# Performance work log

Measured on AMD Instinct MI355X. Metric: run time of the kernel, lower is better.

Reference implementation:

```python
import jax, jax.numpy as jnp
import numpy as np

V, E = 50000, 800000
NODE_IN, EDGE_IN, OUT, HEADS = 128, 16, 32, 4
NEG_SLOPE = 0.2  # DGL EdgeGATConv default negative_slope


def setup_inputs() -> dict:
    key = jax.random.key(0)
    ks = jax.random.split(key, 10)
    return {
        "node_feats": jax.random.normal(ks[0], (V, NODE_IN), jnp.float32),
        "edge_feats": jax.random.normal(ks[1], (E, EDGE_IN), jnp.float32),
        "src": jax.random.randint(ks[2], (E,), 0, V),
        "dst": jax.random.randint(ks[3], (E,), 0, V),
        "W_node": jax.random.normal(ks[4], (NODE_IN, HEADS * OUT), jnp.float32) * 0.05,
        "W_edge": jax.random.normal(ks[5], (EDGE_IN, HEADS * OUT), jnp.float32) * 0.05,
        "attn_l": jax.random.normal(ks[6], (HEADS, OUT), jnp.float32) * 0.05,
        "attn_r": jax.random.normal(ks[7], (HEADS, OUT), jnp.float32) * 0.05,
        "attn_e": jax.random.normal(ks[8], (HEADS, OUT), jnp.float32) * 0.05,
        "res_W": jax.random.normal(ks[9], (NODE_IN, HEADS * OUT), jnp.float32) * 0.05,
        "bias": jnp.zeros((HEADS * OUT,), jnp.float32),
    }


def _leaky_relu(x, slope):
    return jnp.where(x >= 0, x, slope * x)


def reference(node_feats, edge_feats, src, dst, W_node, W_edge, attn_l, attn_r, attn_e, res_W, bias):
    V = node_feats.shape[0]
    H, F = attn_l.shape
    # linear projections
    ft = (node_feats @ W_node).reshape(V, H, F)    # [V,H,F]
    fe = (edge_feats @ W_edge).reshape(-1, H, F)   # [E,H,F]
    # per-head attention logits
    el = jnp.einsum('vhf,hf->vh', ft, attn_l)      # [V,H]
    er = jnp.einsum('vhf,hf->vh', ft, attn_r)      # [V,H]
    ee = jnp.einsum('ehf,hf->eh', fe, attn_e)      # [E,H]
    e = _leaky_relu(el[src] + er[dst] + ee, NEG_SLOPE)  # [E,H]
    # edge softmax over incoming edges of each destination node (stable)
    emax = jax.ops.segment_max(e, dst, num_segments=V)  # [V,H]
    ex = jnp.exp(e - emax[dst])
    esum = jax.ops.segment_sum(ex, dst, num_segments=V)  # [V,H]
    a = ex / esum[dst]                                   # [E,H]
    # weighted message passing: u_mul_e(ft, a) then sum to dst
    msg = ft[src] * a[:, :, None]                        # [E,H,F]
    rst = jax.ops.segment_sum(msg, dst, num_segments=V)  # [V,H,F]
    # residual connection + bias (EdgeGATConv residual=True, bias=True)
    rst = rst + (node_feats @ res_W).reshape(V, H, F)
    rst = rst + bias.reshape(1, H, F)
    # agg_mode='flatten': concat heads
    return rst.reshape(V, H * F)
```

## Files before the change

### kernel.cpp

```cpp
#include <hip/hip_runtime.h>
#include <cstdint>

#define V_N 50000
#define E_N 800000
#define NODE_IN 128
#define EDGE_IN 16
#define HF 128
#define NEG_SLOPE 0.2f
#define NB_SCAN 196

#define OFF_FT    0
#define OFF_EL    3200000
#define OFF_ER    3400000
#define OFF_DEGP  3600000
#define OFF_ROW   4400000
#define OFF_BSUM  4450004
#define OFF_RANK  4450260
#define OFF_REC   5250260
#define OFF_WATT  8450260
#define OFF_BFRAG 8450324

typedef short bf16x8 __attribute__((ext_vector_type(8)));
typedef float f32x4 __attribute__((ext_vector_type(4)));

__device__ __forceinline__ unsigned short f2bf(float f) {
    unsigned u = __float_as_uint(f);
    u += 0x7fffu + ((u >> 16) & 1u);
    return (unsigned short)(u >> 16);
}
__device__ __forceinline__ unsigned pk2(float lo, float hi) {
    return (unsigned)f2bf(lo) | ((unsigned)f2bf(hi) << 16);
}
__device__ __forceinline__ float bflo(unsigned w) { return __uint_as_float(w << 16); }
__device__ __forceinline__ float bfhi(unsigned w) { return __uint_as_float(w & 0xffff0000u); }

__global__ void k_prep(const float* __restrict__ We,
                       const float* __restrict__ attn_e,
                       const float* __restrict__ Wn,
                       const float* __restrict__ Wr,
                       float* __restrict__ watt,
                       unsigned* __restrict__ bfrag) {
    int g = blockIdx.x * 256 + threadIdx.x;
    if (blockIdx.x == 0 && threadIdx.x < 64) {
        int k = threadIdx.x >> 2, h = threadIdx.x & 3;
        float s = 0.f;
        #pragma unroll
        for (int f = 0; f < 32; f++)
            s += We[k * HF + h * 32 + f] * attn_e[h * 32 + f];
        watt[k * 4 + h] = s;
    }
    if (g < 16384) {
        int c    = g >> 8;
        int lane = (g >> 2) & 63;
        int jp   = g & 3;
        int nt = c >> 2, ks = c & 3;
        int col = nt * 16 + (lane & 15);
        int k   = ks * 32 + (lane >> 4) * 8 + jp * 2;
        const float* W = (col < 128) ? Wn : Wr;
        int cc = col & 127;
        float x0 = W[(size_t)k * 128 + cc];
        float x1 = W[(size_t)(k + 1) * 128 + cc];
        bfrag[g] = pk2(x0, x1);
    }
}

__global__ __launch_bounds__(256) void k_node(
    const float* __restrict__ nf, const unsigned* __restrict__ bfragw,
    const float* __restrict__ attn_l, const float* __restrict__ attn_r,
    const float* __restrict__ bias,
    unsigned* __restrict__ ftw, float* __restrict__ el, float* __restrict__ er,
    float* __restrict__ out)
{
    __shared__ __align__(16) float sSf[32 * 140];
    unsigned short* sA = (unsigned short*)sSf;

    const int t = threadIdx.x;
    const int lane = t & 63;
    const int w = t >> 6;
    const int nb = blockIdx.x * 32;
    const int n15 = lane & 15;
    const int q = lane >> 4;
    const unsigned short* bfrag = (const unsigned short*)bfragw;

    #pragma unroll
    for (int i = 0; i < 4; i++) {
        int f = t + i * 256;
        int node = f >> 5;
        int kc = (f & 31) * 4;
        float4 v = {0.f, 0.f, 0.f, 0.f};
        if (nb + node < V_N)
            v = *(const float4*)(nf + (size_t)(nb + node) * NODE_IN + kc);
        uint2 u2 = make_uint2(pk2(v.x, v.y), pk2(v.z, v.w));
        *(uint2*)&sA[node * 136 + kc] = u2;
    }
    __syncthreads();

    f32x4 acc[2][4];
    #pragma unroll
    for (int m = 0; m < 2; m++)
        #pragma unroll
        for (int tt = 0; tt < 4; tt++) acc[m][tt] = (f32x4){0.f, 0.f, 0.f, 0.f};

    #pragma unroll
    for (int ks = 0; ks < 4; ks++) {
        bf16x8 a0 = *(const bf16x8*)&sA[n15 * 136 + ks * 32 + q * 8];
        bf16x8 a1 = *(const bf16x8*)&sA[(16 + n15) * 136 + ks * 32 + q * 8];
        #pragma unroll
        for (int tt = 0; tt < 4; tt++) {
            int nt = w * 4 + tt;
            bf16x8 b = *(const bf16x8*)(bfrag + ((size_t)(nt * 4 + ks) * 64 + lane) * 8);
            acc[0][tt] = __builtin_amdgcn_mfma_f32_16x16x32_bf16(a0, b, acc[0][tt], 0, 0, 0);
            acc[1][tt] = __builtin_amdgcn_mfma_f32_16x16x32_bf16(a1, b, acc[1][tt], 0, 0, 0);
        }
    }

    if (w < 2) {
        #pragma unroll
        for (int hh = 0; hh < 2; hh++) {
            int head = w * 2 + hh;
            float al0 = attn_l[head * 32 + n15];
            float al1 = attn_l[head * 32 + 16 + n15];
            float ar0 = attn_r[head * 32 + n15];
            float ar1 = attn_r[head * 32 + 16 + n15];
            #pragma unroll
            for (int m = 0; m < 2; m++) {
                #pragma unroll
                for (int r = 0; r < 4; r++) {
                    float fa = acc[m][hh * 2][r], fb = acc[m][hh * 2 + 1][r];
                    float elp = fa * al0 + fb * al1;
                    float erp = fa * ar0 + fb * ar1;
                    elp += __shfl_xor(elp, 1); erp += __shfl_xor(erp, 1);
                    elp += __shfl_xor(elp, 2); erp += __shfl_xor(erp, 2);
                    elp += __shfl_xor(elp, 4); erp += __shfl_xor(erp, 4);
                    elp += __shfl_xor(elp, 8); erp += __shfl_xor(erp, 8);
                    int node = nb + m * 16 + q * 4 + r;
                    if (n15 == 0 && node < V_N) {
                        el[node * 4 + head] = elp;
                        er[node * 4 + head] = erp;
                    }
                }
            }
        }
    }
    __syncthreads();

    if (w < 2) {
        #pragma unroll
        for (int m = 0; m < 2; m++)
            #pragma unroll
            for (int tt = 0; tt < 4; tt++)
                #pragma unroll
                for (int r = 0; r < 4; r++)
                    sSf[(m * 16 + q * 4 + r) * 140 + w * 64 + tt * 16 + n15] =
                        acc[m][tt][r];
    }
    __syncthreads();
    #pragma unroll
    for (int i = 0; i < 2; i++) {
        int u = t + i * 256;
        int node = u >> 4, wg = u & 15;
        if (nb + node < V_N) {
            float4 c0 = *(float4*)&sSf[node * 140 + wg * 8];
            float4 c1 = *(float4*)&sSf[node * 140 + wg * 8 + 4];
            uint4 pv = {pk2(c0.x, c0.y), pk2(c0.z, c0.w),
                        pk2(c1.x, c1.y), pk2(c1.z, c1.w)};
            *(uint4*)(ftw + (size_t)(nb + node) * 64 + wg * 4) = pv;
        }
    }
    __syncthreads();

    if (w >= 2) {
        #pragma unroll
        for (int m = 0; m < 2; m++)
            #pragma unroll
            for (int tt = 0; tt < 4; tt++)
                #pragma unroll
                for (int r = 0; r < 4; r++)
                    sSf[(m * 16 + q * 4 + r) * 140 + (w - 2) * 64 + tt * 16 + n15] =
                        acc[m][tt][r];
    }
    __syncthreads();
    #pragma unroll
    for (int i = 0; i < 4; i++) {
        int u = t + i * 256;
        int node = u >> 5, c4 = (u & 31) * 4;
        if (nb + node < V_N) {
            float4 v = *(float4*)&sSf[node * 140 + c4];
            float4 b4 = *(const float4*)(bias + c4);
            v.x += b4.x; v.y += b4.y; v.z += b4.z; v.w += b4.w;
            *(float4*)(out + (size_t)(nb + node) * HF + c4) = v;
        }
    }
}

__global__ void k_hist(const int* __restrict__ dst, int* __restrict__ degp,
                       int* __restrict__ rank) {
    int e = blockIdx.x * 256 + threadIdx.x;
    if (e < E_N) rank[e] = atomicAdd(&degp[(size_t)dst[e] * 16], 1);
}

__global__ __launch_bounds__(256) void k_scan1(const int* __restrict__ degp,
                                               int* __restrict__ rowp,
                                               int* __restrict__ bsum) {
    __shared__ int sh[256];
    int t = threadIdx.x, b = blockIdx.x;
    int i = b * 256 + t;
    int v = (i < V_N) ? degp[(size_t)i * 16] : 0;
    sh[t] = v;
    __syncthreads();
    #pragma unroll
    for (int off = 1; off < 256; off <<= 1) {
        int u = (t >= off) ? sh[t - off] : 0;
        __syncthreads();
        sh[t] += u;
        __syncthreads();
    }
    if (i < V_N) rowp[i] = sh[t] - v;
    if (t == 255) bsum[b] = sh[255];
}

__global__ __launch_bounds__(256) void k_scan23(int* __restrict__ rowp,
                                                const int* __restrict__ bsum) {
    __shared__ int sh[256];
    int t = threadIdx.x, b = blockIdx.x;
    int v = (t < NB_SCAN) ? bsum[t] : 0;
    sh[t] = v;
    __syncthreads();
    #pragma unroll
    for (int off = 1; off < 256; off <<= 1) {
        int u = (t >= off) ? sh[t - off] : 0;
        __syncthreads();
        sh[t] += u;
        __syncthreads();
    }
    int boff = (b == 0) ? 0 : sh[b - 1];
    int i = b * 256 + t;
    if (i < V_N) rowp[i] += boff;
    if (i == 0) rowp[V_N] = E_N;
}

__global__ __launch_bounds__(256) void k_escatter(
    const float* __restrict__ ef, const int* __restrict__ src,
    const int* __restrict__ dst, const int* __restrict__ rank,
    const int* __restrict__ rowp, const float* __restrict__ watt,
    uint4* __restrict__ rec)
{
    __shared__ float sw[64];
    if (threadIdx.x < 64) sw[threadIdx.x] = watt[threadIdx.x];
    __syncthreads();
    int e = blockIdx.x * 256 + threadIdx.x;
    if (e >= E_N) return;

    float eev[4] = {0.f, 0.f, 0.f, 0.f};
    #pragma unroll
    for (int kq = 0; kq < 4; kq++) {
        float4 v = *(const float4*)(ef + (size_t)e * EDGE_IN + kq * 4);
        float vv[4] = {v.x, v.y, v.z, v.w};
        #pragma unroll
        for (int j = 0; j < 4; j++) {
            int k = kq * 4 + j;
            #pragma unroll
            for (int h = 0; h < 4; h++) eev[h] += vv[j] * sw[k * 4 + h];
        }
    }
    int d = dst[e];
    int p = rowp[d] + rank[e];
    uint4 r;
    r.x = (unsigned)src[e];
    r.y = pk2(eev[0], eev[1]);
    r.z = pk2(eev[2], eev[3]);
    r.w = 0;
    rec[p] = r;
}

__global__ __launch_bounds__(256) void k_gather(
    const int* __restrict__ row, const uint4* __restrict__ rec,
    const float* __restrict__ el, const float* __restrict__ er,
    const unsigned* __restrict__ ftw, float* __restrict__ out)
{
    __shared__ float aw[4][64][4];
    const int lane = threadIdx.x & 63;
    const int wid  = threadIdx.x >> 6;
    const int d = blockIdx.x * 4 + wid;
    if (d >= V_N) return;
    const int n0 = row[d];
    const int deg = row[d + 1] - n0;
    if (deg == 0) return;

    float4 er4 = *(const float4*)(er + (size_t)d * 4);

    int   si0 = 0;
    float4 ex0 = {0.f, 0.f, 0.f, 0.f};
    float4 s4  = {0.f, 0.f, 0.f, 0.f};
    for (int i = lane; i < deg; i += 64) {
        uint4 r = rec[n0 + i];
        float4 el4 = *(const float4*)(el + (size_t)r.x * 4);
        float x0 = el4.x + er4.x + bflo(r.y);
        float x1 = el4.y + er4.y + bfhi(r.y);
        float x2 = el4.z + er4.z + bflo(r.z);
        float x3 = el4.w + er4.w + bfhi(r.z);
        x0 = x0 >= 0.f ? x0 : NEG_SLOPE * x0;
        x1 = x1 >= 0.f ? x1 : NEG_SLOPE * x1;
        x2 = x2 >= 0.f ? x2 : NEG_SLOPE * x2;
        x3 = x3 >= 0.f ? x3 : NEG_SLOPE * x3;
        float4 ex = {__expf(x0), __expf(x1), __expf(x2), __expf(x3)};
        if (i == lane) { si0 = (int)r.x; ex0 = ex; }
        s4.x += ex.x; s4.y += ex.y; s4.z += ex.z; s4.w += ex.w;
    }
    #pragma unroll
    for (int off = 1; off < 64; off <<= 1) {
        s4.x += __shfl_xor(s4.x, off);
        s4.y += __shfl_xor(s4.y, off);
        s4.z += __shfl_xor(s4.z, off);
        s4.w += __shfl_xor(s4.w, off);
    }
    float4 rs4 = {1.f / s4.x, 1.f / s4.y, 1.f / s4.z, 1.f / s4.w};

    const int qw = lane >> 4, li = lane & 15, head = li >> 2;
    float acc[8];
    #pragma unroll
    for (int k = 0; k < 8; k++) acc[k] = 0.f;

    for (int i0 = 0; i0 < deg; i0 += 64) {
        int chunk = min(64, deg - i0);
        int si = 0;
        float4 a4 = {0.f, 0.f, 0.f, 0.f};
        if (lane < chunk) {
            if (i0 == 0) {
                si = si0;
                a4.x = ex0.x * rs4.x; a4.y = ex0.y * rs4.y;
                a4.z = ex0.z * rs4.z; a4.w = ex0.w * rs4.w;
            } else {
                uint4 r = rec[n0 + i0 + lane];
                si = (int)r.x;
                float4 el4 = *(const float4*)(el + (size_t)r.x * 4);
                float x0 = el4.x + er4.x + bflo(r.y);
                float x1 = el4.y + er4.y + bfhi(r.y);
                float x2 = el4.z + er4.z + bflo(r.z);
                float x3 = el4.w + er4.w + bfhi(r.z);
                x0 = x0 >= 0.f ? x0 : NEG_SLOPE * x0;
                x1 = x1 >= 0.f ? x1 : NEG_SLOPE * x1;
                x2 = x2 >= 0.f ? x2 : NEG_SLOPE * x2;
                x3 = x3 >= 0.f ? x3 : NEG_SLOPE * x3;
                a4.x = __expf(x0) * rs4.x; a4.y = __expf(x1) * rs4.y;
                a4.z = __expf(x2) * rs4.z; a4.w = __expf(x3) * rs4.w;
            }
        }
        *(float4*)&aw[wid][lane][0] = a4;
        asm volatile("s_waitcnt lgkmcnt(0)" ::: "memory");

        int iters = (chunk + 3) & ~3;
        for (int j = 0; j < iters; j += 4) {
            int jq = j + qw;
            int sidx = __shfl(si, jq);
            float a = aw[wid][jq][head];
            uint4 wv = *(const uint4*)(ftw + (size_t)sidx * 64 + li * 4);
            acc[0] += a * bflo(wv.x); acc[1] += a * bfhi(wv.x);
            acc[2] += a * bflo(wv.y); acc[3] += a * bfhi(wv.y);
            acc[4] += a * bflo(wv.z); acc[5] += a * bfhi(wv.z);
            acc[6] += a * bflo(wv.w); acc[7] += a * bfhi(wv.w);
        }
    }
    #pragma unroll
    for (int k = 0; k < 8; k++) {
        acc[k] += __shfl_xor(acc[k], 16);
        acc[k] += __shfl_xor(acc[k], 32);
    }
    if (qw == 0) {
        float* op = out + (size_t)d * HF + li * 8;
        float4 r0 = *(float4*)op;
        r0.x += acc[0]; r0.y += acc[1]; r0.z += acc[2]; r0.w += acc[3];
        *(float4*)op = r0;
        float4 r1 = *(float4*)(op + 4);
        r1.x += acc[4]; r1.y += acc[5]; r1.z += acc[6]; r1.w += acc[7];
        *(float4*)(op + 4) = r1;
    }
}

extern "C" void kernel_launch(void* const* d_in, const int* in_sizes, int n_in,
                              void* d_out, int out_size, void* d_ws, size_t ws_size,
                              hipStream_t stream) {
    const float* nf     = (const float*)d_in[0];
    const float* ef     = (const float*)d_in[1];
    const int*   src    = (const int*)d_in[2];
    const int*   dst    = (const int*)d_in[3];
    const float* Wn     = (const float*)d_in[4];
    const float* We     = (const float*)d_in[5];
    const float* attn_l = (const float*)d_in[6];
    const float* attn_r = (const float*)d_in[7];
    const float* attn_e = (const float*)d_in[8];
    const float* Wr     = (const float*)d_in[9];
    const float* bias   = (const float*)d_in[10];
    float* out = (float*)d_out;

    unsigned* wsw  = (unsigned*)d_ws;
    unsigned* ftw  = wsw + OFF_FT;
    float* el      = (float*)(wsw + OFF_EL);
    float* er      = (float*)(wsw + OFF_ER);
    int* degp      = (int*)(wsw + OFF_DEGP);
    int* rowp      = (int*)(wsw + OFF_ROW);
    int* bsum      = (int*)(wsw + OFF_BSUM);
    int* rank      = (int*)(wsw + OFF_RANK);
    uint4* rec     = (uint4*)(wsw + OFF_REC);
    float* watt    = (float*)(wsw + OFF_WATT);
    unsigned* bfrag = wsw + OFF_BFRAG;

    hipMemsetAsync(degp, 0, (size_t)V_N * 16 * sizeof(int), stream);

    k_prep<<<64, 256, 0, stream>>>(We, attn_e, Wn, Wr, watt, bfrag);
    k_hist<<<(E_N + 255) / 256, 256, 0, stream>>>(dst, degp, rank);
    k_scan1<<<NB_SCAN, 256, 0, stream>>>(degp, rowp, bsum);
    k_scan23<<<NB_SCAN, 256, 0, stream>>>(rowp, bsum);
    k_escatter<<<(E_N + 255) / 256, 256, 0, stream>>>(ef, src, dst, rank,
                                                      rowp, watt, rec);
    k_node<<<(V_N + 31) / 32, 256, 0, stream>>>(nf, bfrag, attn_l, attn_r,
                                                bias, ftw, el, er, out);
    k_gather<<<(V_N + 3) / 4, 256, 0, stream>>>(rowp, rec, el, er, ftw, out);
}
```

Before: 248.1 us.

## Switch gathered node features to fp16 with packed half2 FMA accumulation

```diff
diff --git a/kernel.cpp b/kernel.cpp
--- a/kernel.cpp
+++ b/kernel.cpp
@@ -1,4 +1,5 @@
 #include <hip/hip_runtime.h>
+#include <hip/hip_fp16.h>
 #include <cstdint>
 
 #define V_N 50000
@@ -12,13 +13,13 @@
 #define OFF_FT    0
 #define OFF_EL    3200000
 #define OFF_ER    3400000
-#define OFF_DEGP  3600000
-#define OFF_ROW   4400000
-#define OFF_BSUM  4450004
-#define OFF_RANK  4450260
-#define OFF_REC   5250260
-#define OFF_WATT  8450260
-#define OFF_BFRAG 8450324
+#define OFF_DEG   3600000
+#define OFF_ROW   3650000
+#define OFF_BSUM  3700004
+#define OFF_RANK  3700260
+#define OFF_REC   4500260
+#define OFF_WATT  7700260
+#define OFF_BFRAG 7700324
 
 typedef short bf16x8 __attribute__((ext_vector_type(8)));
 typedef float f32x4 __attribute__((ext_vector_type(4)));
@@ -33,14 +34,28 @@
 }
 __device__ __forceinline__ float bflo(unsigned w) { return __uint_as_float(w << 16); }
 __device__ __forceinline__ float bfhi(unsigned w) { return __uint_as_float(w & 0xffff0000u); }
+
+typedef __fp16 fp16x2 __attribute__((ext_vector_type(2)));
+__device__ __forceinline__ unsigned pkh2(float a, float b) {
+    fp16x2 h = __builtin_amdgcn_cvt_pkrtz(a, b);
+    return __builtin_bit_cast(unsigned, h);
+}
+__device__ __forceinline__ __half2 u2h(unsigned u) {
+    return __builtin_bit_cast(__half2, u);
+}
+__device__ __forceinline__ unsigned h2u(__half2 h) {
+    return __builtin_bit_cast(unsigned, h);
+}
 
 __global__ void k_prep(const float* __restrict__ We,
                        const float* __restrict__ attn_e,
                        const float* __restrict__ Wn,
                        const float* __restrict__ Wr,
                        float* __restrict__ watt,
-                       unsigned* __restrict__ bfrag) {
+                       unsigned* __restrict__ bfrag,
+                       int* __restrict__ deg) {
     int g = blockIdx.x * 256 + threadIdx.x;
+    for (int i = g; i < V_N; i += 16384) deg[i] = 0;
     if (blockIdx.x == 0 && threadIdx.x < 64) {
         int k = threadIdx.x >> 2, h = threadIdx.x & 3;
         float s = 0.f;
@@ -68,8 +83,8 @@
     const float* __restrict__ nf, const unsigned* __restrict__ bfragw,
     const float* __restrict__ attn_l, const float* __restrict__ attn_r,
     const float* __restrict__ bias,
-    unsigned* __restrict__ ftw, float* __restrict__ el, float* __restrict__ er,
-    float* __restrict__ out)
+    unsigned short* __restrict__ ftw, float* __restrict__ el,
+    float* __restrict__ er, float* __restrict__ out)
 {
     __shared__ __align__(16) float sSf[32 * 140];
     unsigned short* sA = (unsigned short*)sSf;
@@ -141,31 +156,18 @@
                 }
             }
         }
-    }
-    __syncthreads();
-
-    if (w < 2) {
         #pragma unroll
         for (int m = 0; m < 2; m++)
             #pragma unroll
-            for (int tt = 0; tt < 4; tt++)
-                #pragma unroll
-                for (int r = 0; r < 4; r++)
-                    sSf[(m * 16 + q * 4 + r) * 140 + w * 64 + tt * 16 + n15] =
-                        acc[m][tt][r];
-    }
-    __syncthreads();
-    #pragma unroll
-    for (int i = 0; i < 2; i++) {
-        int u = t + i * 256;
-        int node = u >> 4, wg = u & 15;
-        if (nb + node < V_N) {
-            float4 c0 = *(float4*)&sSf[node * 140 + wg * 8];
-            float4 c1 = *(float4*)&sSf[node * 140 + wg * 8 + 4];
-            uint4 pv = {pk2(c0.x, c0.y), pk2(c0.z, c0.w),
-                        pk2(c1.x, c1.y), pk2(c1.z, c1.w)};
-            *(uint4*)(ftw + (size_t)(nb + node) * 64 + wg * 4) = pv;
-        }
+            for (int r = 0; r < 4; r++) {
+                int node = nb + m * 16 + q * 4 + r;
+                if (node < V_N) {
+                    uint2 u;
+                    u.x = pkh2(acc[m][0][r], acc[m][1][r]);
+                    u.y = pkh2(acc[m][2][r], acc[m][3][r]);
+                    *(uint2*)(ftw + (size_t)node * 128 + w * 64 + n15 * 4) = u;
+                }
+            }
     }
     __syncthreads();
 
@@ -193,19 +195,19 @@
     }
 }
 
-__global__ void k_hist(const int* __restrict__ dst, int* __restrict__ degp,
+__global__ void k_hist(const int* __restrict__ dst, int* __restrict__ deg,
                        int* __restrict__ rank) {
     int e = blockIdx.x * 256 + threadIdx.x;
-    if (e < E_N) rank[e] = atomicAdd(&degp[(size_t)dst[e] * 16], 1);
-}
-
-__global__ __launch_bounds__(256) void k_scan1(const int* __restrict__ degp,
+    if (e < E_N) rank[e] = atomicAdd(&deg[dst[e]], 1);
+}
+
+__global__ __launch_bounds__(256) void k_scan1(const int* __restrict__ deg,
                                                int* __restrict__ rowp,
                                                int* __restrict__ bsum) {
     __shared__ int sh[256];
     int t = threadIdx.x, b = blockIdx.x;
     int i = b * 256 + t;
-    int v = (i < V_N) ? degp[(size_t)i * 16] : 0;
+    int v = (i < V_N) ? deg[i] : 0;
     sh[t] = v;
     __syncthreads();
     #pragma unroll
@@ -276,9 +278,9 @@
 __global__ __launch_bounds__(256) void k_gather(
     const int* __restrict__ row, const uint4* __restrict__ rec,
     const float* __restrict__ el, const float* __restrict__ er,
-    const unsigned* __restrict__ ftw, float* __restrict__ out)
+    const unsigned short* __restrict__ ftw, float* __restrict__ out)
 {
-    __shared__ float aw[4][64][4];
+    __shared__ unsigned aw[4][64][4];
     const int lane = threadIdx.x & 63;
     const int wid  = threadIdx.x >> 6;
     const int d = blockIdx.x * 4 + wid;
@@ -316,10 +318,9 @@
     }
     float4 rs4 = {1.f / s4.x, 1.f / s4.y, 1.f / s4.z, 1.f / s4.w};
 
-    const int qw = lane >> 4, li = lane & 15, head = li >> 2;
-    float acc[8];
-    #pragma unroll
-    for (int k = 0; k < 8; k++) acc[k] = 0.f;
+    const int qw = lane >> 4, li = lane & 15;
+    const int wsel = li >> 3;
+    __half2 hacc0 = u2h(0u), hacc1 = u2h(0u), hacc2 = u2h(0u), hacc3 = u2h(0u);
 
     for (int i0 = 0; i0 < deg; i0 += 64) {
         int chunk = min(64, deg - i0);
@@ -346,34 +347,39 @@
                 a4.z = __expf(x2) * rs4.z; a4.w = __expf(x3) * rs4.w;
             }
         }
-        *(float4*)&aw[wid][lane][0] = a4;
+        uint4 ap;
+        ap.x = pkh2(a4.x, a4.x); ap.y = pkh2(a4.y, a4.y);
+        ap.z = pkh2(a4.z, a4.z); ap.w = pkh2(a4.w, a4.w);
+        *(uint4*)&aw[wid][lane][0] = ap;
         asm volatile("s_waitcnt lgkmcnt(0)" ::: "memory");
 
         int iters = (chunk + 3) & ~3;
         for (int j = 0; j < iters; j += 4) {
             int jq = j + qw;
             int sidx = __shfl(si, jq);
-            float a = aw[wid][jq][head];
-            uint4 wv = *(const uint4*)(ftw + (size_t)sidx * 64 + li * 4);
-            acc[0] += a * bflo(wv.x); acc[1] += a * bfhi(wv.x);
-            acc[2] += a * bflo(wv.y); acc[3] += a * bfhi(wv.y);
-            acc[4] += a * bflo(wv.z); acc[5] += a * bfhi(wv.z);
-            acc[6] += a * bflo(wv.w); acc[7] += a * bfhi(wv.w);
-        }
-    }
-    #pragma unroll
-    for (int k = 0; k < 8; k++) {
-        acc[k] += __shfl_xor(acc[k], 16);
-        acc[k] += __shfl_xor(acc[k], 32);
-    }
+            uint2 au = *(const uint2*)&aw[wid][jq][wsel * 2];
+            uint4 wv = *(const uint4*)(ftw + (size_t)sidx * 128 + li * 8);
+            hacc0 = __hfma2(u2h(wv.x), u2h(au.x), hacc0);
+            hacc1 = __hfma2(u2h(wv.y), u2h(au.y), hacc1);
+            hacc2 = __hfma2(u2h(wv.z), u2h(au.x), hacc2);
+            hacc3 = __hfma2(u2h(wv.w), u2h(au.y), hacc3);
+        }
+    }
+    hacc0 = __hadd2(hacc0, u2h(__shfl_xor(h2u(hacc0), 16)));
+    hacc1 = __hadd2(hacc1, u2h(__shfl_xor(h2u(hacc1), 16)));
+    hacc2 = __hadd2(hacc2, u2h(__shfl_xor(h2u(hacc2), 16)));
+    hacc3 = __hadd2(hacc3, u2h(__shfl_xor(h2u(hacc3), 16)));
+    hacc0 = __hadd2(hacc0, u2h(__shfl_xor(h2u(hacc0), 32)));
+    hacc1 = __hadd2(hacc1, u2h(__shfl_xor(h2u(hacc1), 32)));
+    hacc2 = __hadd2(hacc2, u2h(__shfl_xor(h2u(hacc2), 32)));
+    hacc3 = __hadd2(hacc3, u2h(__shfl_xor(h2u(hacc3), 32)));
     if (qw == 0) {
-        float* op = out + (size_t)d * HF + li * 8;
-        float4 r0 = *(float4*)op;
-        r0.x += acc[0]; r0.y += acc[1]; r0.z += acc[2]; r0.w += acc[3];
-        *(float4*)op = r0;
-        float4 r1 = *(float4*)(op + 4);
-        r1.x += acc[4]; r1.y += acc[5]; r1.z += acc[6]; r1.w += acc[7];
-        *(float4*)(op + 4) = r1;
+        float* op = out + (size_t)d * HF + wsel * 64 + (li & 7) * 2;
+        float2 r;
+        r = *(float2*)(op +  0); r.x += __low2float(hacc0);  r.y += __low2float(hacc2);  *(float2*)(op +  0) = r;
+        r = *(float2*)(op + 16); r.x += __high2float(hacc0); r.y += __high2float(hacc2); *(float2*)(op + 16) = r;
+        r = *(float2*)(op + 32); r.x += __low2float(hacc1);  r.y += __low2float(hacc3);  *(float2*)(op + 32) = r;
+        r = *(float2*)(op + 48); r.x += __high2float(hacc1); r.y += __high2float(hacc3); *(float2*)(op + 48) = r;
     }
 }
 
@@ -394,10 +400,10 @@
     float* out = (float*)d_out;
 
     unsigned* wsw  = (unsigned*)d_ws;
-    unsigned* ftw  = wsw + OFF_FT;
+    unsigned short* ftw = (unsigned short*)(wsw + OFF_FT);
     float* el      = (float*)(wsw + OFF_EL);
     float* er      = (float*)(wsw + OFF_ER);
-    int* degp      = (int*)(wsw + OFF_DEGP);
+    int* deg       = (int*)(wsw + OFF_DEG);
     int* rowp      = (int*)(wsw + OFF_ROW);
     int* bsum      = (int*)(wsw + OFF_BSUM);
     int* rank      = (int*)(wsw + OFF_RANK);
@@ -405,11 +411,9 @@
     float* watt    = (float*)(wsw + OFF_WATT);
     unsigned* bfrag = wsw + OFF_BFRAG;
 
-    hipMemsetAsync(degp, 0, (size_t)V_N * 16 * sizeof(int), stream);
-
-    k_prep<<<64, 256, 0, stream>>>(We, attn_e, Wn, Wr, watt, bfrag);
-    k_hist<<<(E_N + 255) / 256, 256, 0, stream>>>(dst, degp, rank);
-    k_scan1<<<NB_SCAN, 256, 0, stream>>>(degp, rowp, bsum);
+    k_prep<<<64, 256, 0, stream>>>(We, attn_e, Wn, Wr, watt, bfrag, deg);
+    k_hist<<<(E_N + 255) / 256, 256, 0, stream>>>(dst, deg, rank);
+    k_scan1<<<NB_SCAN, 256, 0, stream>>>(deg, rowp, bsum);
     k_scan23<<<NB_SCAN, 256, 0, stream>>>(rowp, bsum);
     k_escatter<<<(E_N + 255) / 256, 256, 0, stream>>>(ef, src, dst, rank,
                                                       rowp, watt, rec);
```

Result: no change. 248.9 us (+0.3%).
